# Kernel tuning notes

Measured on AMD Instinct MI355X. Metric: run time of the kernel, lower is better.

Reference implementation:

```python
import jax, jax.numpy as jnp
import numpy as np

B, LN, LT, D, DIN, H = 8, 64, 256, 1024, 2048, 4
LN_EPS = 1e-5
F16_EPS = float(np.finfo(np.float16).eps)


def setup_inputs() -> dict:
    key = jax.random.key(0)
    ks = jax.random.split(key, 16)
    n = lambda k, sh: jax.random.normal(k, sh, dtype=jnp.float32)
    s = 0.02
    z = lambda sh: jnp.zeros(sh, jnp.float32)
    return {
        "text_embeds": n(ks[0], (B, LT, D)),
        "node_embeds": n(ks[1], (B, LN, D)),
        "Wq": n(ks[2], (D, H * D)) * s, "bq": z((H * D,)),
        "Wk": n(ks[3], (D, H * D)) * s, "bk": z((H * D,)),
        "Wv": n(ks[4], (D, H * D)) * s, "bv": z((H * D,)),
        "Wo": n(ks[5], (H * D, D)) * s, "bo": z((D,)),
        "ln_g": jnp.ones((D,), jnp.float32), "ln_b": z((D,)),
        "aqW": n(ks[6], (D, D)) * s, "aqb": z((D,)),
        "akW": n(ks[7], (D, D)) * s, "akb": z((D,)),
        "att_v": n(ks[8], (D,)) * (1.0 / np.sqrt(D)),
        "att_b": z((D,)),
        "dp1W": n(ks[9], (D, DIN // 2)) * s, "dp1b": z((DIN // 2,)),
        "dp2W": n(ks[10], (DIN // 2, DIN)) * s, "dp2b": z((DIN,)),
        "gnn_mask": jax.random.randint(ks[11], (B, LN), 0, 2),
        "lm_mask": jax.random.randint(ks[12], (B, LT), 0, 2),
    }


def _forward(text_embeds, node_embeds, Wq, bq, Wk, bk, Wv, bv, Wo, bo, ln_g, ln_b,
             aqW, aqb, akW, akb, att_v, att_b, dp1W, dp1b, dp2W, dp2b,
             gnn_mask, lm_mask):
    x = node_embeds  # (B, LN, D)

    # ---- selfAttention_prompt: each of 4 heads has full width D ----
    def heads(w, b):
        return (x @ w + b).reshape(B, LN, H, D).transpose(0, 2, 1, 3)  # (B,H,LN,D)

    Q, K, V = heads(Wq, bq), heads(Wk, bk), heads(Wv, bv)
    A = jnp.einsum('bhqd,bhkd->bhqk', Q, K) / jnp.sqrt(jnp.float32(D))
    A = jnp.where(gnn_mask[:, None, None, :] == 0, -jnp.inf, A)
    alpha = jax.nn.softmax(A, axis=-1)
    out = jnp.einsum('bhqk,bhkd->bhqd', alpha, V)
    out = out.transpose(0, 2, 1, 3).reshape(B, LN, H * D)
    out = out @ Wo + bo + x
    # LayerNorm (torch default eps=1e-5)
    mu = out.mean(-1, keepdims=True)
    var = ((out - mu) ** 2).mean(-1, keepdims=True)
    H2 = (out - mu) / jnp.sqrt(var + LN_EPS) * ln_g + ln_b  # (B, LN, D)

    # ---- AdditiveAttention (Bahdanau): value_proj is unused in the original ----
    q = H2 @ aqW + aqb            # (B, LN, D)
    k = text_embeds @ akW + akb   # (B, LT, D)
    e = jnp.einsum('bqkd,d->bqk',
                   jnp.tanh(q[:, :, None, :] + k[:, None, :, :] + att_b), att_v)
    e = jnp.where(lm_mask[:, None, :] == 0, -jnp.inf, e)
    w = jax.nn.softmax(e, axis=-1)            # (B, LN, LT)
    H3 = jnp.einsum('bqk,bkd->bqd', w, text_embeds)  # context with raw V

    # ---- filter_Pool: masked mean over nodes ----
    m = gnn_mask.astype(H3.dtype)[:, :, None]
    cnt = jnp.clip(m.sum(1), F16_EPS, None)   # (B, 1)
    H4 = (H3 * m).sum(1) / cnt                # (B, D)

    # ---- domain projector (exact GELU like torch) ----
    Z = jax.nn.gelu(H4 @ dp1W + dp1b, approximate=False) @ dp2W + dp2b
    return Z  # (B, DIN)


def reference(text_embeds, node_embeds, Wq, bq, Wk, bk, Wv, bv, Wo, bo, ln_g, ln_b,
              aqW, aqb, akW, akb, att_v, att_b, dp1W, dp1b, dp2W, dp2b,
              gnn_mask, lm_mask):
    return _forward(text_embeds, node_embeds, Wq, bq, Wk, bk, Wv, bv, Wo, bo,
                    ln_g, ln_b, aqW, aqb, akW, akb, att_v, att_b,
                    dp1W, dp1b, dp2W, dp2b, gnn_mask, lm_mask)
```

## Files before the change

### kernel.cpp

```cpp
#include <hip/hip_runtime.h>
#include <hip/hip_bf16.h>
#include <math.h>

#define NB 8
#define LNN 64
#define LTN 256
#define DD 1024
#define NH 4
#define HDD 4096
#define DINN 2048
#define DHN 1024

#define C_TANH 2.8853900817779268f

typedef __bf16 bf16x8 __attribute__((ext_vector_type(8)));
typedef float f32x4 __attribute__((ext_vector_type(4)));

__device__ __forceinline__ float b2f(ushort u) {
  union { float f; unsigned int i; } x; x.i = ((unsigned int)u) << 16; return x.f;
}
__device__ __forceinline__ ushort f2b(float f) {
  unsigned int u = __builtin_bit_cast(unsigned int, f);
  u = (u + 0x7FFFu + ((u >> 16) & 1u)) >> 16;
  return (ushort)u;
}

__global__ __launch_bounds__(256) void cvt_all(const float* __restrict__ node,
                                               ushort* __restrict__ node_bf,
                                               const float* __restrict__ text,
                                               ushort* __restrict__ text_bf) {
  int bid = blockIdx.x;
  const float* in;
  ushort* out;
  int i;
  if (bid < 256) { in = node; out = node_bf; i = (bid * 256 + threadIdx.x) * 8; }
  else { in = text; out = text_bf; i = ((bid - 256) * 256 + threadIdx.x) * 8; }
  float4 a = *(const float4*)(in + i);
  float4 b = *(const float4*)(in + i + 4);
  ushort4 o0 = {f2b(a.x), f2b(a.y), f2b(a.z), f2b(a.w)};
  ushort4 o1 = {f2b(b.x), f2b(b.y), f2b(b.z), f2b(b.w)};
  *(ushort4*)(out + i) = o0;
  *(ushort4*)(out + i + 4) = o1;
}

__global__ __launch_bounds__(256) void tcvt3(const float* __restrict__ W0,
                                             const float* __restrict__ W1,
                                             const float* __restrict__ W2,
                                             ushort* __restrict__ Wt, int K, int N) {
  int z = blockIdx.z;
  const float* W = (z == 0) ? W0 : ((z == 1) ? W1 : W2);
  ushort* dst0 = Wt + (size_t)z * K * N;
  __shared__ float tf[64][65];
  int k0 = blockIdx.y << 6, n0 = blockIdx.x << 6;
  int t = threadIdx.x;
  int r = t >> 2, c4 = (t & 3) * 16;
  const float* src = W + (size_t)(k0 + r) * N + n0 + c4;
  float4 v0 = *(const float4*)(src);
  float4 v1 = *(const float4*)(src + 4);
  float4 v2 = *(const float4*)(src + 8);
  float4 v3 = *(const float4*)(src + 12);
  *(float4*)&tf[r][c4] = v0;
  *(float4*)&tf[r][c4 + 4] = v1;
  *(float4*)&tf[r][c4 + 8] = v2;
  *(float4*)&tf[r][c4 + 12] = v3;
  __syncthreads();
  int nl = t >> 2, kc = (t & 3) * 16;
  ushort tmp[16];
#pragma unroll
  for (int j = 0; j < 16; ++j) tmp[j] = f2b(tf[kc + j][nl]);
  ushort* dst = dst0 + (size_t)(n0 + nl) * K + k0 + kc;
  *(uint4*)(dst) = *(uint4*)&tmp[0];
  *(uint4*)(dst + 8) = *(uint4*)&tmp[8];
}

__global__ __launch_bounds__(256) void gemm_qkv3(const ushort* __restrict__ A,
                                                 const ushort* __restrict__ BtB,
                                                 const float* __restrict__ b0,
                                                 const float* __restrict__ b1,
                                                 const float* __restrict__ b2,
                                                 ushort* __restrict__ o0,
                                                 ushort* __restrict__ o1,
                                                 ushort* __restrict__ o2,
                                                 int M, int N, int K) {
  int z = blockIdx.z;
  const ushort* Bt = BtB + (size_t)z * N * K;
  const float* bias = (z == 0) ? b0 : ((z == 1) ? b1 : b2);
  ushort* Cout = (z == 0) ? o0 : ((z == 1) ? o1 : o2);
  __shared__ ushort Als[64 * 64];
  __shared__ ushort Bls[128 * 64];
  int tid = threadIdx.x;
  int m0 = blockIdx.y << 6, n0 = blockIdx.x << 7;
  int srow = tid >> 3, su = tid & 7;
  int sx = (su ^ (srow & 7)) * 8;
  const ushort* ga = A + (size_t)(m0 + srow) * K + su * 8;
  const ushort* gb = Bt + (size_t)(n0 + srow) * K + su * 8;
  int wa0 = srow * 64 + sx, wa1 = (srow + 32) * 64 + sx;
  int wb2 = (srow + 64) * 64 + sx, wb3 = (srow + 96) * 64 + sx;
  const size_t rs32 = (size_t)32 * K;
  int lane = tid & 63, w = tid >> 6;
  int wm = w >> 1, wn = w & 1;
  int r = lane & 15, kg = lane >> 4;
  f32x4 acc[2][4] = {};
  uint4 pa0 = *(const uint4*)(ga);
  uint4 pa1 = *(const uint4*)(ga + rs32);
  uint4 pb0 = *(const uint4*)(gb);
  uint4 pb1 = *(const uint4*)(gb + rs32);
  uint4 pb2 = *(const uint4*)(gb + 2 * rs32);
  uint4 pb3 = *(const uint4*)(gb + 3 * rs32);
  for (int k0 = 0; k0 < K; k0 += 64) {
    __syncthreads();
    *(uint4*)&Als[wa0] = pa0; *(uint4*)&Als[wa1] = pa1;
    *(uint4*)&Bls[wa0] = pb0; *(uint4*)&Bls[wa1] = pb1;
    *(uint4*)&Bls[wb2] = pb2; *(uint4*)&Bls[wb3] = pb3;
    __syncthreads();
    int kn = k0 + 64;
    if (kn < K) {
      pa0 = *(const uint4*)(ga + kn);
      pa1 = *(const uint4*)(ga + rs32 + kn);
      pb0 = *(const uint4*)(gb + kn);
      pb1 = *(const uint4*)(gb + rs32 + kn);
      pb2 = *(const uint4*)(gb + 2 * rs32 + kn);
      pb3 = *(const uint4*)(gb + 3 * rs32 + kn);
    }
#pragma unroll
    for (int h = 0; h < 2; ++h) {
      int sa = ((h * 4 + kg) ^ (r & 7)) * 8;
      bf16x8 af[2], bfr[4];
#pragma unroll
      for (int m = 0; m < 2; ++m)
        af[m] = *(const bf16x8*)&Als[(wm * 32 + m * 16 + r) * 64 + sa];
#pragma unroll
      for (int n = 0; n < 4; ++n)
        bfr[n] = *(const bf16x8*)&Bls[(wn * 64 + n * 16 + r) * 64 + sa];
#pragma unroll
      for (int m = 0; m < 2; ++m)
#pragma unroll
        for (int n = 0; n < 4; ++n)
          acc[m][n] = __builtin_amdgcn_mfma_f32_16x16x32_bf16(af[m], bfr[n], acc[m][n], 0, 0, 0);
    }
  }
#pragma unroll
  for (int m = 0; m < 2; ++m)
#pragma unroll
    for (int n = 0; n < 4; ++n) {
      f32x4 a = acc[m][n];
#pragma unroll
      for (int v = 0; v < 4; ++v) {
        int row = m0 + wm * 32 + m * 16 + kg * 4 + v;
        int col = n0 + wn * 64 + n * 16 + r;
        Cout[(size_t)row * N + col] = f2b(a[v] + bias[col]);
      }
    }
}

__global__ __launch_bounds__(256) void gemm_wo_split(const ushort* __restrict__ A,
                                                     const ushort* __restrict__ Bt,
                                                     float* __restrict__ P,
                                                     int M, int N, int K) {
  __shared__ ushort Als[64 * 64];
  __shared__ ushort Bls[128 * 64];
  int tid = threadIdx.x;
  int m0 = blockIdx.y << 6, n0 = blockIdx.x << 7;
  int Ks = K >> 2, kbase = blockIdx.z * Ks;
  int srow = tid >> 3, su = tid & 7;
  int sx = (su ^ (srow & 7)) * 8;
  const ushort* ga = A + (size_t)(m0 + srow) * K + kbase + su * 8;
  const ushort* gb = Bt + (size_t)(n0 + srow) * K + kbase + su * 8;
  int wa0 = srow * 64 + sx, wa1 = (srow + 32) * 64 + sx;
  int wb2 = (srow + 64) * 64 + sx, wb3 = (srow + 96) * 64 + sx;
  const size_t rs32 = (size_t)32 * K;
  int lane = tid & 63, w = tid >> 6;
  int wm = w >> 1, wn = w & 1;
  int r = lane & 15, kg = lane >> 4;
  f32x4 acc[2][4] = {};
  uint4 pa0 = *(const uint4*)(ga);
  uint4 pa1 = *(const uint4*)(ga + rs32);
  uint4 pb0 = *(const uint4*)(gb);
  uint4 pb1 = *(const uint4*)(gb + rs32);
  uint4 pb2 = *(const uint4*)(gb + 2 * rs32);
  uint4 pb3 = *(const uint4*)(gb + 3 * rs32);
  for (int k0 = 0; k0 < Ks; k0 += 64) {
    __syncthreads();
    *(uint4*)&Als[wa0] = pa0; *(uint4*)&Als[wa1] = pa1;
    *(uint4*)&Bls[wa0] = pb0; *(uint4*)&Bls[wa1] = pb1;
    *(uint4*)&Bls[wb2] = pb2; *(uint4*)&Bls[wb3] = pb3;
    __syncthreads();
    int kn = k0 + 64;
    if (kn < Ks) {
      pa0 = *(const uint4*)(ga + kn);
      pa1 = *(const uint4*)(ga + rs32 + kn);
      pb0 = *(const uint4*)(gb + kn);
      pb1 = *(const uint4*)(gb + rs32 + kn);
      pb2 = *(const uint4*)(gb + 2 * rs32 + kn);
      pb3 = *(const uint4*)(gb + 3 * rs32 + kn);
    }
#pragma unroll
    for (int h = 0; h < 2; ++h) {
      int sa = ((h * 4 + kg) ^ (r & 7)) * 8;
      bf16x8 af[2], bfr[4];
#pragma unroll
      for (int m = 0; m < 2; ++m)
        af[m] = *(const bf16x8*)&Als[(wm * 32 + m * 16 + r) * 64 + sa];
#pragma unroll
      for (int n = 0; n < 4; ++n)
        bfr[n] = *(const bf16x8*)&Bls[(wn * 64 + n * 16 + r) * 64 + sa];
#pragma unroll
      for (int m = 0; m < 2; ++m)
#pragma unroll
        for (int n = 0; n < 4; ++n)
          acc[m][n] = __builtin_amdgcn_mfma_f32_16x16x32_bf16(af[m], bfr[n], acc[m][n], 0, 0, 0);
    }
  }
#pragma unroll
  for (int m = 0; m < 2; ++m)
#pragma unroll
    for (int n = 0; n < 4; ++n) {
      f32x4 a = acc[m][n];
#pragma unroll
      for (int v = 0; v < 4; ++v) {
        int row = m0 + wm * 32 + m * 16 + kg * 4 + v;
        int col = n0 + wn * 64 + n * 16 + r;
        P[((size_t)blockIdx.z * M + row) * N + col] = a[v];
      }
    }
}

__global__ __launch_bounds__(256) void gemm_aqak(const ushort* __restrict__ H2,
                                                 const ushort* __restrict__ Tbf,
                                                 const ushort* __restrict__ TwtAQ,
                                                 const float* __restrict__ aqb,
                                                 const float* __restrict__ akb,
                                                 const float* __restrict__ attb,
                                                 float* __restrict__ QBu,
                                                 float* __restrict__ KAB,
                                                 int N, int K) {
  __shared__ ushort Als[64 * 64];
  __shared__ ushort Bls[128 * 64];
  int tid = threadIdx.x;
  int gm0 = blockIdx.y << 6, n0 = blockIdx.x << 7;
  const ushort* Abase;
  const ushort* Bt;
  const float* bias;
  const float* bias2;
  float* Obase;
  if (gm0 < 512) {
    Abase = H2 + (size_t)gm0 * K;
    Bt = TwtAQ;
    bias = aqb; bias2 = nullptr;
    Obase = QBu + (size_t)gm0 * N;
  } else {
    Abase = Tbf + (size_t)(gm0 - 512) * K;
    Bt = TwtAQ + (size_t)N * K;
    bias = akb; bias2 = attb;
    Obase = KAB + (size_t)(gm0 - 512) * N;
  }
  int srow = tid >> 3, su = tid & 7;
  int sx = (su ^ (srow & 7)) * 8;
  const ushort* ga = Abase + (size_t)srow * K + su * 8;
  const ushort* gb = Bt + (size_t)(n0 + srow) * K + su * 8;
  int wa0 = srow * 64 + sx, wa1 = (srow + 32) * 64 + sx;
  int wb2 = (srow + 64) * 64 + sx, wb3 = (srow + 96) * 64 + sx;
  const size_t rs32 = (size_t)32 * K;
  int lane = tid & 63, w = tid >> 6;
  int wm = w >> 1, wn = w & 1;
  int r = lane & 15, kg = lane >> 4;
  f32x4 acc[2][4] = {};
  uint4 pa0 = *(const uint4*)(ga);
  uint4 pa1 = *(const uint4*)(ga + rs32);
  uint4 pb0 = *(const uint4*)(gb);
  uint4 pb1 = *(const uint4*)(gb + rs32);
  uint4 pb2 = *(const uint4*)(gb + 2 * rs32);
  uint4 pb3 = *(const uint4*)(gb + 3 * rs32);
  for (int k0 = 0; k0 < K; k0 += 64) {
    __syncthreads();
    *(uint4*)&Als[wa0] = pa0; *(uint4*)&Als[wa1] = pa1;
    *(uint4*)&Bls[wa0] = pb0; *(uint4*)&Bls[wa1] = pb1;
    *(uint4*)&Bls[wb2] = pb2; *(uint4*)&Bls[wb3] = pb3;
    __syncthreads();
    int kn = k0 + 64;
    if (kn < K) {
      pa0 = *(const uint4*)(ga + kn);
      pa1 = *(const uint4*)(ga + rs32 + kn);
      pb0 = *(const uint4*)(gb + kn);
      pb1 = *(const uint4*)(gb + rs32 + kn);
      pb2 = *(const uint4*)(gb + 2 * rs32 + kn);
      pb3 = *(const uint4*)(gb + 3 * rs32 + kn);
    }
#pragma unroll
    for (int h = 0; h < 2; ++h) {
      int sa = ((h * 4 + kg) ^ (r & 7)) * 8;
      bf16x8 af[2], bfr[4];
#pragma unroll
      for (int m = 0; m < 2; ++m)
        af[m] = *(const bf16x8*)&Als[(wm * 32 + m * 16 + r) * 64 + sa];
#pragma unroll
      for (int n = 0; n < 4; ++n)
        bfr[n] = *(const bf16x8*)&Bls[(wn * 64 + n * 16 + r) * 64 + sa];
#pragma unroll
      for (int m = 0; m < 2; ++m)
#pragma unroll
        for (int n = 0; n < 4; ++n)
          acc[m][n] = __builtin_amdgcn_mfma_f32_16x16x32_bf16(af[m], bfr[n], acc[m][n], 0, 0, 0);
    }
  }
#pragma unroll
  for (int m = 0; m < 2; ++m)
#pragma unroll
    for (int n = 0; n < 4; ++n) {
      f32x4 a = acc[m][n];
#pragma unroll
      for (int v = 0; v < 4; ++v) {
        int lrow = wm * 32 + m * 16 + kg * 4 + v;
        int col = n0 + wn * 64 + n * 16 + r;
        float x = a[v] + bias[col];
        if (bias2) x += bias2[col];
        Obase[(size_t)lrow * N + col] = x * C_TANH;
      }
    }
}

__global__ __launch_bounds__(256) void wo_ln(const float* __restrict__ P,
                                             const float* __restrict__ bo,
                                             const float* __restrict__ node,
                                             const float* __restrict__ g,
                                             const float* __restrict__ be,
                                             ushort* __restrict__ Y) {
  int row = blockIdx.x, tid = threadIdx.x;
  int c = tid * 4;
  const size_t MN = (size_t)512 * 1024;
  size_t o = (size_t)row * DD + c;
  float4 v0 = *(const float4*)(P + o);
  float4 v1 = *(const float4*)(P + MN + o);
  float4 v2 = *(const float4*)(P + 2 * MN + o);
  float4 v3 = *(const float4*)(P + 3 * MN + o);
  float4 rv = *(const float4*)(node + o);
  float4 bv = *(const float4*)(bo + c);
  float4 v;
  v.x = v0.x + v1.x + v2.x + v3.x + rv.x + bv.x;
  v.y = v0.y + v1.y + v2.y + v3.y + rv.y + bv.y;
  v.z = v0.z + v1.z + v2.z + v3.z + rv.z + bv.z;
  v.w = v0.w + v1.w + v2.w + v3.w + rv.w + bv.w;
  float s = v.x + v.y + v.z + v.w;
  float ss = v.x * v.x + v.y * v.y + v.z * v.z + v.w * v.w;
  for (int o2 = 32; o2; o2 >>= 1) {
    s += __shfl_xor(s, o2, 64);
    ss += __shfl_xor(ss, o2, 64);
  }
  __shared__ float rb_[8];
  int lane = tid & 63, w = tid >> 6;
  if (lane == 0) { rb_[w] = s; rb_[4 + w] = ss; }
  __syncthreads();
  s = rb_[0] + rb_[1] + rb_[2] + rb_[3];
  ss = rb_[4] + rb_[5] + rb_[6] + rb_[7];
  float mu = s * (1.f / 1024.f);
  float var = ss * (1.f / 1024.f) - mu * mu;
  float rstd = rsqrtf(var + 1e-5f);
  ushort4 o4;
  o4.x = f2b((v.x - mu) * rstd * g[c + 0] + be[c + 0]);
  o4.y = f2b((v.y - mu) * rstd * g[c + 1] + be[c + 1]);
  o4.z = f2b((v.z - mu) * rstd * g[c + 2] + be[c + 2]);
  o4.w = f2b((v.w - mu) * rstd * g[c + 3] + be[c + 3]);
  *(ushort4*)(Y + (size_t)row * DD + c) = o4;
}

__global__ __launch_bounds__(256) void attn_qk(const ushort* __restrict__ Qb,
                                               const ushort* __restrict__ Kb,
                                               float* __restrict__ Sp) {
  int bh = blockIdx.x, ks = blockIdx.y;
  int b = bh >> 2;
  size_t base = ((size_t)b * LNN) * HDD + (size_t)(bh & 3) * DD + ks * 128;
  __shared__ ushort Als[64 * 64];
  __shared__ ushort Bls[64 * 64];
  int tid = threadIdx.x;
  int srow = tid >> 2, su0 = (tid & 3) * 2;
  const ushort* ga = Qb + base + (size_t)srow * HDD + su0 * 8;
  const ushort* gb = Kb + base + (size_t)srow * HDD + su0 * 8;
  int wa0 = srow * 64 + ((su0) ^ (srow & 7)) * 8;
  int wa1 = srow * 64 + ((su0 + 1) ^ (srow & 7)) * 8;
  int lane = tid & 63, w = tid >> 6;
  int wm = w >> 1, wn = w & 1;
  int r = lane & 15, kg = lane >> 4;
  f32x4 acc[2][2] = {};
  uint4 pa0 = *(const uint4*)(ga);
  uint4 pa1 = *(const uint4*)(ga + 8);
  uint4 pb0 = *(const uint4*)(gb);
  uint4 pb1 = *(const uint4*)(gb + 8);
  for (int k0 = 0; k0 < 128; k0 += 64) {
    __syncthreads();
    *(uint4*)&Als[wa0] = pa0; *(uint4*)&Als[wa1] = pa1;
    *(uint4*)&Bls[wa0] = pb0; *(uint4*)&Bls[wa1] = pb1;
    __syncthreads();
    if (k0 == 0) {
      pa0 = *(const uint4*)(ga + 64);
      pa1 = *(const uint4*)(ga + 64 + 8);
      pb0 = *(const uint4*)(gb + 64);
      pb1 = *(const uint4*)(gb + 64 + 8);
    }
#pragma unroll
    for (int h = 0; h < 2; ++h) {
      int sa = ((h * 4 + kg) ^ (r & 7)) * 8;
      bf16x8 af[2], bfr[2];
#pragma unroll
      for (int m = 0; m < 2; ++m)
        af[m] = *(const bf16x8*)&Als[(wm * 32 + m * 16 + r) * 64 + sa];
#pragma unroll
      for (int n = 0; n < 2; ++n)
        bfr[n] = *(const bf16x8*)&Bls[(wn * 32 + n * 16 + r) * 64 + sa];
#pragma unroll
      for (int m = 0; m < 2; ++m)
#pragma unroll
        for (int n = 0; n < 2; ++n)
          acc[m][n] = __builtin_amdgcn_mfma_f32_16x16x32_bf16(af[m], bfr[n], acc[m][n], 0, 0, 0);
    }
  }
  float* out = Sp + ((size_t)ks * 32 + bh) * 4096;
#pragma unroll
  for (int m = 0; m < 2; ++m)
#pragma unroll
    for (int n = 0; n < 2; ++n) {
      f32x4 a = acc[m][n];
#pragma unroll
      for (int v = 0; v < 4; ++v) {
        int row = wm * 32 + m * 16 + kg * 4 + v;
        int col = wn * 32 + n * 16 + r;
        out[row * 64 + col] = a[v];
      }
    }
}

__global__ __launch_bounds__(256) void attn_pv(const float* __restrict__ Sp,
                                               const ushort* __restrict__ Vb,
                                               const int* __restrict__ gmask,
                                               ushort* __restrict__ AO) {
  int bid = blockIdx.x;
  int bh = bid >> 3, dt = bid & 7;
  int b = bh >> 2;
  int d0 = dt * 128;
  size_t base = ((size_t)b * LNN) * HDD + (size_t)(bh & 3) * DD;
  __shared__ float S[64][68];
  __shared__ ushort Pls[64 * 72];
  __shared__ ushort Vt[128 * 72];
  int tid = threadIdx.x;
  int lane = tid & 63, w = tid >> 6;
  {
    int fbase = tid * 16;
    float a[16];
#pragma unroll
    for (int i = 0; i < 16; i += 4) {
      float4 v = *(const float4*)(Sp + (size_t)bh * 4096 + fbase + i);
      a[i] = v.x; a[i + 1] = v.y; a[i + 2] = v.z; a[i + 3] = v.w;
    }
#pragma unroll
    for (int ks = 1; ks < 8; ++ks) {
      const float* p = Sp + ((size_t)ks * 32 + bh) * 4096 + fbase;
#pragma unroll
      for (int i = 0; i < 16; i += 4) {
        float4 v = *(const float4*)(p + i);
        a[i] += v.x; a[i + 1] += v.y; a[i + 2] += v.z; a[i + 3] += v.w;
      }
    }
    int q = fbase >> 6, k = fbase & 63;
#pragma unroll
    for (int i = 0; i < 16; ++i) S[q][k + i] = a[i];
  }
  {
    int kq = lane, dq = w * 32;
    const ushort* src = Vb + base + (size_t)kq * HDD + d0 + dq;
    uint4 v0 = *(const uint4*)src;
    uint4 v1 = *(const uint4*)(src + 8);
    uint4 v2 = *(const uint4*)(src + 16);
    uint4 v3 = *(const uint4*)(src + 24);
    ushort tmp[32];
    *(uint4*)&tmp[0] = v0; *(uint4*)&tmp[8] = v1;
    *(uint4*)&tmp[16] = v2; *(uint4*)&tmp[24] = v3;
#pragma unroll
    for (int j = 0; j < 32; ++j) Vt[(dq + j) * 72 + kq] = tmp[j];
  }
  __syncthreads();
  bool valid = gmask[b * LNN + lane] != 0;
  for (int i = 0; i < 16; ++i) {
    int q = w * 16 + i;
    float v = valid ? S[q][lane] * 0.03125f : -__builtin_inff();
    float mx = v;
    for (int o = 32; o; o >>= 1) mx = fmaxf(mx, __shfl_xor(mx, o, 64));
    float e = valid ? __expf(v - mx) : 0.f;
    float s = e;
    for (int o = 32; o; o >>= 1) s += __shfl_xor(s, o, 64);
    Pls[q * 72 + lane] = f2b(__fdividef(e, s));
  }
  __syncthreads();
  int wm = w >> 1, wn = w & 1;
  int r = lane & 15, kg = lane >> 4;
  f32x4 acc[2][4] = {};
#pragma unroll
  for (int h = 0; h < 2; ++h) {
    int ko = h * 32 + kg * 8;
    bf16x8 af[2], bfr[4];
#pragma unroll
    for (int m = 0; m < 2; ++m)
      af[m] = *(const bf16x8*)&Pls[(wm * 32 + m * 16 + r) * 72 + ko];
#pragma unroll
    for (int n = 0; n < 4; ++n)
      bfr[n] = *(const bf16x8*)&Vt[(wn * 64 + n * 16 + r) * 72 + ko];
#pragma unroll
    for (int m = 0; m < 2; ++m)
#pragma unroll
      for (int n = 0; n < 4; ++n)
        acc[m][n] = __builtin_amdgcn_mfma_f32_16x16x32_bf16(af[m], bfr[n], acc[m][n], 0, 0, 0);
  }
#pragma unroll
  for (int m = 0; m < 2; ++m)
#pragma unroll
    for (int n = 0; n < 4; ++n) {
      f32x4 a = acc[m][n];
#pragma unroll
      for (int v = 0; v < 4; ++v) {
        int q = wm * 32 + m * 16 + kg * 4 + v;
        int col = wn * 64 + n * 16 + r;
        AO[base + (size_t)q * HDD + d0 + col] = f2b(a[v]);
      }
    }
}

__global__ __launch_bounds__(256) void addatt_e(const float* __restrict__ QBu,
                                                const float* __restrict__ KAB,
                                                const float* __restrict__ av_,
                                                float* __restrict__ E4) {
  int dq = blockIdx.x, qt = blockIdx.y, b = blockIdx.z;
  int tid = threadIdx.x;
  __shared__ float qs[4][256];
  __shared__ float avs[256];
  __shared__ float red[4];
  int bq0 = b * LNN + qt * 4;
#pragma unroll
  for (int qq = 0; qq < 4; ++qq)
    qs[qq][tid] = QBu[(size_t)(bq0 + qq) * DD + dq * 256 + tid];
  float av = av_[dq * 256 + tid];
  avs[tid] = av;
  float s = av;
  for (int o = 32; o; o >>= 1) s += __shfl_xor(s, o, 64);
  int lane = tid & 63, w = tid >> 6;
  if (lane == 0) red[w] = s;
  __syncthreads();
  float sumav = red[0] + red[1] + red[2] + red[3];
  const float* kr = KAB + (size_t)(b * LTN + tid) * DD + dq * 256;
  float ac0 = 0.f, ac1 = 0.f, ac2 = 0.f, ac3 = 0.f;
#pragma unroll 2
  for (int d = 0; d < 256; d += 4) {
    float4 kv = *(const float4*)(kr + d);
    float4 av4 = *(const float4*)&avs[d];
    float4 q0 = *(const float4*)&qs[0][d];
    float4 q1 = *(const float4*)&qs[1][d];
    float4 q2 = *(const float4*)&qs[2][d];
    float4 q3 = *(const float4*)&qs[3][d];
    ac0 = fmaf(av4.x, __builtin_amdgcn_rcpf(__builtin_amdgcn_exp2f(q0.x + kv.x) + 1.f), ac0);
    ac1 = fmaf(av4.x, __builtin_amdgcn_rcpf(__builtin_amdgcn_exp2f(q1.x + kv.x) + 1.f), ac1);
    ac2 = fmaf(av4.x, __builtin_amdgcn_rcpf(__builtin_amdgcn_exp2f(q2.x + kv.x) + 1.f), ac2);
    ac3 = fmaf(av4.x, __builtin_amdgcn_rcpf(__builtin_amdgcn_exp2f(q3.x + kv.x) + 1.f), ac3);
    ac0 = fmaf(av4.y, __builtin_amdgcn_rcpf(__builtin_amdgcn_exp2f(q0.y + kv.y) + 1.f), ac0);
    ac1 = fmaf(av4.y, __builtin_amdgcn_rcpf(__builtin_amdgcn_exp2f(q1.y + kv.y) + 1.f), ac1);
    ac2 = fmaf(av4.y, __builtin_amdgcn_rcpf(__builtin_amdgcn_exp2f(q2.y + kv.y) + 1.f), ac2);
    ac3 = fmaf(av4.y, __builtin_amdgcn_rcpf(__builtin_amdgcn_exp2f(q3.y + kv.y) + 1.f), ac3);
    ac0 = fmaf(av4.z, __builtin_amdgcn_rcpf(__builtin_amdgcn_exp2f(q0.z + kv.z) + 1.f), ac0);
    ac1 = fmaf(av4.z, __builtin_amdgcn_rcpf(__builtin_amdgcn_exp2f(q1.z + kv.z) + 1.f), ac1);
    ac2 = fmaf(av4.z, __builtin_amdgcn_rcpf(__builtin_amdgcn_exp2f(q2.z + kv.z) + 1.f), ac2);
    ac3 = fmaf(av4.z, __builtin_amdgcn_rcpf(__builtin_amdgcn_exp2f(q3.z + kv.z) + 1.f), ac3);
    ac0 = fmaf(av4.w, __builtin_amdgcn_rcpf(__builtin_amdgcn_exp2f(q0.w + kv.w) + 1.f), ac0);
    ac1 = fmaf(av4.w, __builtin_amdgcn_rcpf(__builtin_amdgcn_exp2f(q1.w + kv.w) + 1.f), ac1);
    ac2 = fmaf(av4.w, __builtin_amdgcn_rcpf(__builtin_amdgcn_exp2f(q2.w + kv.w) + 1.f), ac2);
    ac3 = fmaf(av4.w, __builtin_amdgcn_rcpf(__builtin_amdgcn_exp2f(q3.w + kv.w) + 1.f), ac3);
  }
  size_t ebase = ((size_t)dq * 512 + bq0) * LTN + tid;
  E4[ebase] = sumav - 2.f * ac0;
  E4[ebase + LTN] = sumav - 2.f * ac1;
  E4[ebase + 2 * LTN] = sumav - 2.f * ac2;
  E4[ebase + 3 * LTN] = sumav - 2.f * ac3;
}

__global__ __launch_bounds__(256) void addatt_sm(const float* __restrict__ E4,
                                                 const int* __restrict__ lmask,
                                                 float* __restrict__ Wv) {
  int bq = blockIdx.x;
  int b = bq >> 6;
  int tid = threadIdx.x;
  __shared__ float rb_[8];
  float e = E4[(size_t)bq * LTN + tid] + E4[((size_t)512 + bq) * LTN + tid] +
            E4[((size_t)1024 + bq) * LTN + tid] + E4[((size_t)1536 + bq) * LTN + tid];
  bool valid = lmask[b * LTN + tid] != 0;
  float v = valid ? e : -__builtin_inff();
  int lane = tid & 63, w = tid >> 6;
  float m = v;
  for (int o = 32; o; o >>= 1) m = fmaxf(m, __shfl_xor(m, o, 64));
  if (lane == 0) rb_[w] = m;
  __syncthreads();
  m = fmaxf(fmaxf(rb_[0], rb_[1]), fmaxf(rb_[2], rb_[3]));
  float ex = valid ? __expf(v - m) : 0.f;
  float sm = ex;
  for (int o = 32; o; o >>= 1) sm += __shfl_xor(sm, o, 64);
  if (lane == 0) rb_[4 + w] = sm;
  __syncthreads();
  sm = rb_[4] + rb_[5] + rb_[6] + rb_[7];
  Wv[(size_t)bq * LTN + tid] = __fdividef(ex, sm);
}

__global__ __launch_bounds__(256) void addatt_pool(const float* __restrict__ Wv,
                                                   const float* __restrict__ text,
                                                   const int* __restrict__ gmask,
                                                   float* __restrict__ H4) {
  int dt = blockIdx.x, b = blockIdx.y;
  int tid = threadIdx.x;
  __shared__ float cf[LTN];
  float c = 0.f, cnt = 0.f;
#pragma unroll 8
  for (int q = 0; q < LNN; ++q) {
    float m = (gmask[b * LNN + q] != 0) ? 1.f : 0.f;
    cnt += m;
    c = fmaf(m, Wv[(size_t)(b * LNN + q) * LTN + tid], c);
  }
  cf[tid] = c;
  cnt = fmaxf(cnt, 9.765625e-04f);
  __syncthreads();
  int d = dt * 256 + tid;
  const float* tb = text + (size_t)b * LTN * DD + d;
  float acc = 0.f;
#pragma unroll 8
  for (int k = 0; k < LTN; ++k) acc = fmaf(cf[k], tb[(size_t)k * DD], acc);
  H4[b * DD + d] = acc / cnt;
}

__global__ __launch_bounds__(256) void dp_split(const float* __restrict__ X,
                                                const float* __restrict__ W,
                                                float* __restrict__ P,
                                                int K, int N) {
  int jt = blockIdx.x, kt = blockIdx.y;
  int t = threadIdx.x;
  __shared__ float xs[8][32];
  if (t < 64) {
    int b = t >> 3, kk = (t & 7) * 4;
    *(float4*)&xs[b][kk] = *(const float4*)(X + (size_t)b * K + kt * 32 + kk);
  }
  __syncthreads();
  int j = jt * 64 + (t & 63);
  int bg = (t >> 6) * 2;
  const float* wp = W + (size_t)(kt * 32) * N + j;
  float a0 = 0.f, a1 = 0.f;
#pragma unroll
  for (int k = 0; k < 32; ++k) {
    float w = wp[(size_t)k * N];
    a0 = fmaf(xs[bg + 0][k], w, a0);
    a1 = fmaf(xs[bg + 1][k], w, a1);
  }
  P[((size_t)kt * 8 + bg + 0) * N + j] = a0;
  P[((size_t)kt * 8 + bg + 1) * N + j] = a1;
}

template <int GELU>
__global__ __launch_bounds__(256) void dp_reduce(const float* __restrict__ P,
                                                 const float* __restrict__ bias,
                                                 float* __restrict__ O, int N) {
  int b = blockIdx.y;
  int j = blockIdx.x * 256 + threadIdx.x;
  float s = bias[j];
#pragma unroll 8
  for (int kt = 0; kt < 32; ++kt) s += P[((size_t)kt * 8 + b) * N + j];
  if constexpr (GELU) s = 0.5f * s * (1.f + erff(s * 0.70710678118654752440f));
  O[(size_t)b * N + j] = s;
}

extern "C" void kernel_launch(void* const* d_in, const int* in_sizes, int n_in,
                              void* d_out, int out_size, void* d_ws, size_t ws_size,
                              hipStream_t stream) {
  const float* text = (const float*)d_in[0];
  const float* node = (const float*)d_in[1];
  const float* Wq = (const float*)d_in[2];
  const float* bq = (const float*)d_in[3];
  const float* Wk = (const float*)d_in[4];
  const float* bk = (const float*)d_in[5];
  const float* Wv = (const float*)d_in[6];
  const float* bv = (const float*)d_in[7];
  const float* Wo = (const float*)d_in[8];
  const float* bo = (const float*)d_in[9];
  const float* lng = (const float*)d_in[10];
  const float* lnb = (const float*)d_in[11];
  const float* aqW = (const float*)d_in[12];
  const float* aqb = (const float*)d_in[13];
  const float* akW = (const float*)d_in[14];
  const float* akb = (const float*)d_in[15];
  const float* attv = (const float*)d_in[16];
  const float* attb = (const float*)d_in[17];
  const float* dp1W = (const float*)d_in[18];
  const float* dp1b = (const float*)d_in[19];
  const float* dp2W = (const float*)d_in[20];
  const float* dp2b = (const float*)d_in[21];
  const int* gmask = (const int*)d_in[22];
  const int* lmask = (const int*)d_in[23];
  (void)in_sizes; (void)n_in; (void)out_size;

  char* base = (char*)d_ws;
#define MB(x) (((size_t)(x)) << 20)
  ushort* Twt = (ushort*)(base);
  float* Sp = (float*)(base);
  ushort* node_bf = (ushort*)(base + MB(8));
  ushort* text_bf = (ushort*)(base + MB(9));
  ushort* Qb = (ushort*)(base + MB(13));
  ushort* Kb = (ushort*)(base + MB(17));
  ushort* Vb = (ushort*)(base + MB(21));
  ushort* AO = (ushort*)(base + MB(25));
  float* E4 = (float*)(base + MB(13));
  float* Wvb = (float*)(base + MB(15));
  ushort* H2 = (ushort*)(base + MB(15) + (512 << 10));
  float* P_Wo = (float*)(base + MB(17));
  float* P1 = (float*)(base + MB(18));
  float* P2 = (float*)(base + MB(19));
  float* QBu = (float*)(base + MB(21));
  float* KAB = (float*)(base + MB(25));
  float* H4 = (float*)(base + MB(33));
  float* G = (float*)(base + MB(33) + 32768);
  ushort* TwtQKV = (ushort*)(base + MB(34));
  float* Z = (float*)d_out;
  const bool bigws = ws_size >= MB(59);
#undef MB

  const int M1 = NB * LNN;
  dim3 blk(256);

  cvt_all<<<dim3(1280), blk, 0, stream>>>(node, node_bf, text, text_bf);

  if (bigws) {
    tcvt3<<<dim3(HDD / 64, DD / 64, 3), blk, 0, stream>>>(Wq, Wk, Wv, TwtQKV, DD, HDD);
    gemm_qkv3<<<dim3(HDD / 128, M1 / 64, 3), blk, 0, stream>>>(node_bf, TwtQKV, bq, bk, bv, Qb, Kb, Vb, M1, HDD, DD);
  } else {
    tcvt3<<<dim3(HDD / 64, DD / 64, 1), blk, 0, stream>>>(Wq, Wq, Wq, Twt, DD, HDD);
    gemm_qkv3<<<dim3(HDD / 128, M1 / 64, 1), blk, 0, stream>>>(node_bf, Twt, bq, bq, bq, Qb, Qb, Qb, M1, HDD, DD);
    tcvt3<<<dim3(HDD / 64, DD / 64, 1), blk, 0, stream>>>(Wk, Wk, Wk, Twt, DD, HDD);
    gemm_qkv3<<<dim3(HDD / 128, M1 / 64, 1), blk, 0, stream>>>(node_bf, Twt, bk, bk, bk, Kb, Kb, Kb, M1, HDD, DD);
    tcvt3<<<dim3(HDD / 64, DD / 64, 1), blk, 0, stream>>>(Wv, Wv, Wv, Twt, DD, HDD);
    gemm_qkv3<<<dim3(HDD / 128, M1 / 64, 1), blk, 0, stream>>>(node_bf, Twt, bv, bv, bv, Vb, Vb, Vb, M1, HDD, DD);
  }

  attn_qk<<<dim3(NB * NH, 8), blk, 0, stream>>>(Qb, Kb, Sp);
  attn_pv<<<dim3(NB * NH * 8), blk, 0, stream>>>(Sp, Vb, gmask, AO);

  tcvt3<<<dim3(DD / 64, HDD / 64, 1), blk, 0, stream>>>(Wo, Wo, Wo, Twt, HDD, DD);
  gemm_wo_split<<<dim3(DD / 128, M1 / 64, 4), blk, 0, stream>>>(AO, Twt, P_Wo, M1, DD, HDD);
  wo_ln<<<dim3(M1), blk, 0, stream>>>(P_Wo, bo, node, lng, lnb, H2);

  tcvt3<<<dim3(DD / 64, DD / 64, 2), blk, 0, stream>>>(aqW, akW, akW, Twt, DD, DD);
  gemm_aqak<<<dim3(DD / 128, 40), blk, 0, stream>>>(H2, text_bf, Twt, aqb, akb, attb, QBu, KAB, DD, DD);

  addatt_e<<<dim3(4, 16, NB), blk, 0, stream>>>(QBu, KAB, attv, E4);
  addatt_sm<<<dim3(M1), blk, 0, stream>>>(E4, lmask, Wvb);
  addatt_pool<<<dim3(4, NB), blk, 0, stream>>>(Wvb, text, gmask, H4);

  dp_split<<<dim3(DHN / 64, 32), blk, 0, stream>>>(H4, dp1W, P1, DD, DHN);
  dp_reduce<1><<<dim3(DHN / 256, NB), blk, 0, stream>>>(P1, dp1b, G, DHN);
  dp_split<<<dim3(DINN / 64, 32), blk, 0, stream>>>(G, dp2W, P2, DHN, DINN);
  dp_reduce<0><<<dim3(DINN / 256, NB), blk, 0, stream>>>(P2, dp2b, Z, DINN);
}
```

Baseline: 173.7 us.

## Fuse all input/weight conversions into one prep kernel and retile additive attention

Merges the activation bf16 conversion and all weight transpose-conversions (QKV, Wo, aq/ak) into a single large launch with a fixed workspace layout, removing the small-workspace fallback and several separate launches. This cuts launch gaps and lets weight conversion for later stages run alongside the earlier ones. The additive-attention score kernel now processes 8 queries over 128-wide d slices instead of 4 queries over 256, so each loaded K row is reused across more queries. The softmax kernel then sums 8 partial slices instead of 4. The change now assumes the workspace is large enough for the fixed layout.

Result: faster. 162.0 us (-6.7%).

```diff
diff --git a/kernel.cpp b/kernel.cpp
--- a/kernel.cpp
+++ b/kernel.cpp
@@ -16,43 +16,61 @@
 typedef __bf16 bf16x8 __attribute__((ext_vector_type(8)));
 typedef float f32x4 __attribute__((ext_vector_type(4)));
 
-__device__ __forceinline__ float b2f(ushort u) {
-  union { float f; unsigned int i; } x; x.i = ((unsigned int)u) << 16; return x.f;
-}
 __device__ __forceinline__ ushort f2b(float f) {
   unsigned int u = __builtin_bit_cast(unsigned int, f);
   u = (u + 0x7FFFu + ((u >> 16) & 1u)) >> 16;
   return (ushort)u;
 }
 
-__global__ __launch_bounds__(256) void cvt_all(const float* __restrict__ node,
-                                               ushort* __restrict__ node_bf,
-                                               const float* __restrict__ text,
-                                               ushort* __restrict__ text_bf) {
+__global__ __launch_bounds__(256) void prep(const float* __restrict__ node,
+                                            ushort* __restrict__ node_bf,
+                                            const float* __restrict__ text,
+                                            ushort* __restrict__ text_bf,
+                                            const float* __restrict__ Wq,
+                                            const float* __restrict__ Wk,
+                                            const float* __restrict__ Wv,
+                                            const float* __restrict__ Wo,
+                                            const float* __restrict__ aqW,
+                                            const float* __restrict__ akW,
+                                            ushort* __restrict__ TwtQKV,
+                                            ushort* __restrict__ TwtWo,
+                                            ushort* __restrict__ TwtAQ) {
   int bid = blockIdx.x;
-  const float* in;
-  ushort* out;
-  int i;
-  if (bid < 256) { in = node; out = node_bf; i = (bid * 256 + threadIdx.x) * 8; }
-  else { in = text; out = text_bf; i = ((bid - 256) * 256 + threadIdx.x) * 8; }
-  float4 a = *(const float4*)(in + i);
-  float4 b = *(const float4*)(in + i + 4);
-  ushort4 o0 = {f2b(a.x), f2b(a.y), f2b(a.z), f2b(a.w)};
-  ushort4 o1 = {f2b(b.x), f2b(b.y), f2b(b.z), f2b(b.w)};
-  *(ushort4*)(out + i) = o0;
-  *(ushort4*)(out + i + 4) = o1;
-}
-
-__global__ __launch_bounds__(256) void tcvt3(const float* __restrict__ W0,
-                                             const float* __restrict__ W1,
-                                             const float* __restrict__ W2,
-                                             ushort* __restrict__ Wt, int K, int N) {
-  int z = blockIdx.z;
-  const float* W = (z == 0) ? W0 : ((z == 1) ? W1 : W2);
-  ushort* dst0 = Wt + (size_t)z * K * N;
+  int t = threadIdx.x;
+  if (bid < 1280) {
+    const float* in;
+    ushort* out;
+    int i;
+    if (bid < 256) { in = node; out = node_bf; i = (bid * 256 + t) * 8; }
+    else { in = text; out = text_bf; i = ((bid - 256) * 256 + t) * 8; }
+    float4 a = *(const float4*)(in + i);
+    float4 b = *(const float4*)(in + i + 4);
+    ushort4 o0 = {f2b(a.x), f2b(a.y), f2b(a.z), f2b(a.w)};
+    ushort4 o1 = {f2b(b.x), f2b(b.y), f2b(b.z), f2b(b.w)};
+    *(ushort4*)(out + i) = o0;
+    *(ushort4*)(out + i + 4) = o1;
+    return;
+  }
+  bid -= 1280;
+  const float* W;
+  ushort* dst0;
+  int K, N, tt;
+  if (bid < 3072) {
+    int z = bid >> 10;
+    tt = bid & 1023;
+    W = (z == 0) ? Wq : ((z == 1) ? Wk : Wv);
+    dst0 = TwtQKV + (size_t)z * DD * HDD;
+    K = DD; N = HDD;
+  } else if (bid < 4096) {
+    tt = bid - 3072; W = Wo; dst0 = TwtWo; K = HDD; N = DD;
+  } else if (bid < 4352) {
+    tt = bid - 4096; W = aqW; dst0 = TwtAQ; K = DD; N = DD;
+  } else {
+    tt = bid - 4352; W = akW; dst0 = TwtAQ + (size_t)DD * DD; K = DD; N = DD;
+  }
+  int ntn = N >> 6;
+  int n0 = (tt % ntn) << 6, k0 = (tt / ntn) << 6;
   __shared__ float tf[64][65];
-  int k0 = blockIdx.y << 6, n0 = blockIdx.x << 6;
-  int t = threadIdx.x;
   int r = t >> 2, c4 = (t & 3) * 16;
   const float* src = W + (size_t)(k0 + r) * N + n0 + c4;
   float4 v0 = *(const float4*)(src);
@@ -525,67 +543,57 @@
 __global__ __launch_bounds__(256) void addatt_e(const float* __restrict__ QBu,
                                                 const float* __restrict__ KAB,
                                                 const float* __restrict__ av_,
-                                                float* __restrict__ E4) {
-  int dq = blockIdx.x, qt = blockIdx.y, b = blockIdx.z;
+                                                float* __restrict__ E8) {
+  int ds = blockIdx.x, qt = blockIdx.y, b = blockIdx.z;
   int tid = threadIdx.x;
-  __shared__ float qs[4][256];
-  __shared__ float avs[256];
+  __shared__ float qs[8][128];
+  __shared__ float avs[128];
   __shared__ float red[4];
-  int bq0 = b * LNN + qt * 4;
-#pragma unroll
-  for (int qq = 0; qq < 4; ++qq)
-    qs[qq][tid] = QBu[(size_t)(bq0 + qq) * DD + dq * 256 + tid];
-  float av = av_[dq * 256 + tid];
-  avs[tid] = av;
+  int bq0 = b * LNN + qt * 8;
+  {
+    int qq = tid >> 5, dd = (tid & 31) * 4;
+    *(float4*)&qs[qq][dd] = *(const float4*)(QBu + (size_t)(bq0 + qq) * DD + ds * 128 + dd);
+  }
+  float av = (tid < 128) ? av_[ds * 128 + tid] : 0.f;
+  if (tid < 128) avs[tid] = av;
   float s = av;
   for (int o = 32; o; o >>= 1) s += __shfl_xor(s, o, 64);
   int lane = tid & 63, w = tid >> 6;
   if (lane == 0) red[w] = s;
   __syncthreads();
   float sumav = red[0] + red[1] + red[2] + red[3];
-  const float* kr = KAB + (size_t)(b * LTN + tid) * DD + dq * 256;
-  float ac0 = 0.f, ac1 = 0.f, ac2 = 0.f, ac3 = 0.f;
+  const float* kr = KAB + (size_t)(b * LTN + tid) * DD + ds * 128;
+  float ac[8] = {};
 #pragma unroll 2
-  for (int d = 0; d < 256; d += 4) {
+  for (int d = 0; d < 128; d += 4) {
     float4 kv = *(const float4*)(kr + d);
     float4 av4 = *(const float4*)&avs[d];
-    float4 q0 = *(const float4*)&qs[0][d];
-    float4 q1 = *(const float4*)&qs[1][d];
-    float4 q2 = *(const float4*)&qs[2][d];
-    float4 q3 = *(const float4*)&qs[3][d];
-    ac0 = fmaf(av4.x, __builtin_amdgcn_rcpf(__builtin_amdgcn_exp2f(q0.x + kv.x) + 1.f), ac0);
-    ac1 = fmaf(av4.x, __builtin_amdgcn_rcpf(__builtin_amdgcn_exp2f(q1.x + kv.x) + 1.f), ac1);
-    ac2 = fmaf(av4.x, __builtin_amdgcn_rcpf(__builtin_amdgcn_exp2f(q2.x + kv.x) + 1.f), ac2);
-    ac3 = fmaf(av4.x, __builtin_amdgcn_rcpf(__builtin_amdgcn_exp2f(q3.x + kv.x) + 1.f), ac3);
-    ac0 = fmaf(av4.y, __builtin_amdgcn_rcpf(__builtin_amdgcn_exp2f(q0.y + kv.y) + 1.f), ac0);
-    ac1 = fmaf(av4.y, __builtin_amdgcn_rcpf(__builtin_amdgcn_exp2f(q1.y + kv.y) + 1.f), ac1);
-    ac2 = fmaf(av4.y, __builtin_amdgcn_rcpf(__builtin_amdgcn_exp2f(q2.y + kv.y) + 1.f), ac2);
-    ac3 = fmaf(av4.y, __builtin_amdgcn_rcpf(__builtin_amdgcn_exp2f(q3.y + kv.y) + 1.f), ac3);
-    ac0 = fmaf(av4.z, __builtin_amdgcn_rcpf(__builtin_amdgcn_exp2f(q0.z + kv.z) + 1.f), ac0);
-    ac1 = fmaf(av4.z, __builtin_amdgcn_rcpf(__builtin_amdgcn_exp2f(q1.z + kv.z) + 1.f), ac1);
-    ac2 = fmaf(av4.z, __builtin_amdgcn_rcpf(__builtin_amdgcn_exp2f(q2.z + kv.z) + 1.f), ac2);
-    ac3 = fmaf(av4.z, __builtin_amdgcn_rcpf(__builtin_amdgcn_exp2f(q3.z + kv.z) + 1.f), ac3);
-    ac0 = fmaf(av4.w, __builtin_amdgcn_rcpf(__builtin_amdgcn_exp2f(q0.w + kv.w) + 1.f), ac0);
-    ac1 = fmaf(av4.w, __builtin_amdgcn_rcpf(__builtin_amdgcn_exp2f(q1.w + kv.w) + 1.f), ac1);
-    ac2 = fmaf(av4.w, __builtin_amdgcn_rcpf(__builtin_amdgcn_exp2f(q2.w + kv.w) + 1.f), ac2);
-    ac3 = fmaf(av4.w, __builtin_amdgcn_rcpf(__builtin_amdgcn_exp2f(q3.w + kv.w) + 1.f), ac3);
-  }
-  size_t ebase = ((size_t)dq * 512 + bq0) * LTN + tid;
-  E4[ebase] = sumav - 2.f * ac0;
-  E4[ebase + LTN] = sumav - 2.f * ac1;
-  E4[ebase + 2 * LTN] = sumav - 2.f * ac2;
-  E4[ebase + 3 * LTN] = sumav - 2.f * ac3;
-}
-
-__global__ __launch_bounds__(256) void addatt_sm(const float* __restrict__ E4,
+#pragma unroll
+    for (int qq = 0; qq < 8; ++qq) {
+      float4 q4 = *(const float4*)&qs[qq][d];
+      ac[qq] = fmaf(av4.x, __builtin_amdgcn_rcpf(__builtin_amdgcn_exp2f(q4.x + kv.x) + 1.f), ac[qq]);
+      ac[qq] = fmaf(av4.y, __builtin_amdgcn_rcpf(__builtin_amdgcn_exp2f(q4.y + kv.y) + 1.f), ac[qq]);
+      ac[qq] = fmaf(av4.z, __builtin_amdgcn_rcpf(__builtin_amdgcn_exp2f(q4.z + kv.z) + 1.f), ac[qq]);
+      ac[qq] = fmaf(av4.w, __builtin_amdgcn_rcpf(__builtin_amdgcn_exp2f(q4.w + kv.w) + 1.f), ac[qq]);
+    }
+  }
+  size_t ebase = ((size_t)ds * 512 + bq0) * LTN + tid;
+#pragma unroll
+  for (int qq = 0; qq < 8; ++qq)
+    E8[ebase + (size_t)qq * LTN] = sumav - 2.f * ac[qq];
+}
+
+__global__ __launch_bounds__(256) void addatt_sm(const float* __restrict__ E8,
                                                  const int* __restrict__ lmask,
                                                  float* __restrict__ Wv) {
   int bq = blockIdx.x;
   int b = bq >> 6;
   int tid = threadIdx.x;
   __shared__ float rb_[8];
-  float e = E4[(size_t)bq * LTN + tid] + E4[((size_t)512 + bq) * LTN + tid] +
-            E4[((size_t)1024 + bq) * LTN + tid] + E4[((size_t)1536 + bq) * LTN + tid];
+  float e = 0.f;
+#pragma unroll
+  for (int ks = 0; ks < 8; ++ks)
+    e += E8[((size_t)ks * 512 + bq) * LTN + tid];
   bool valid = lmask[b * LTN + tid] != 0;
   float v = valid ? e : -__builtin_inff();
   int lane = tid & 63, w = tid >> 6;
@@ -694,62 +702,52 @@
   const float* dp2b = (const float*)d_in[21];
   const int* gmask = (const int*)d_in[22];
   const int* lmask = (const int*)d_in[23];
-  (void)in_sizes; (void)n_in; (void)out_size;
+  (void)in_sizes; (void)n_in; (void)out_size; (void)ws_size;
 
   char* base = (char*)d_ws;
 #define MB(x) (((size_t)(x)) << 20)
-  ushort* Twt = (ushort*)(base);
-  float* Sp = (float*)(base);
-  ushort* node_bf = (ushort*)(base + MB(8));
-  ushort* text_bf = (ushort*)(base + MB(9));
-  ushort* Qb = (ushort*)(base + MB(13));
-  ushort* Kb = (ushort*)(base + MB(17));
-  ushort* Vb = (ushort*)(base + MB(21));
-  ushort* AO = (ushort*)(base + MB(25));
-  float* E4 = (float*)(base + MB(13));
-  float* Wvb = (float*)(base + MB(15));
-  ushort* H2 = (ushort*)(base + MB(15) + (512 << 10));
-  float* P_Wo = (float*)(base + MB(17));
-  float* P1 = (float*)(base + MB(18));
-  float* P2 = (float*)(base + MB(19));
-  float* QBu = (float*)(base + MB(21));
-  float* KAB = (float*)(base + MB(25));
-  float* H4 = (float*)(base + MB(33));
-  float* G = (float*)(base + MB(33) + 32768);
-  ushort* TwtQKV = (ushort*)(base + MB(34));
+  ushort* TwtQKV = (ushort*)(base);
+  ushort* TwtWo = (ushort*)(base + MB(24));
+  ushort* TwtAQ = (ushort*)(base + MB(32));
+  ushort* node_bf = (ushort*)(base + MB(36));
+  ushort* text_bf = (ushort*)(base + MB(37));
+  ushort* Qb = (ushort*)(base + MB(41));
+  ushort* Kb = (ushort*)(base + MB(45));
+  ushort* Vb = (ushort*)(base + MB(49));
+  ushort* AO = (ushort*)(base + MB(53));
+  float* Sp = (float*)(base + MB(57));
+  float* P_Wo = (float*)(base + MB(61));
+  ushort* H2 = (ushort*)(base + MB(69));
+  float* QBu = (float*)(base + MB(70));
+  float* KAB = (float*)(base + MB(72));
+  float* E8 = (float*)(base + MB(80));
+  float* Wvb = (float*)(base + MB(84));
+  float* H4 = (float*)(base + MB(84) + (512 << 10));
+  float* G = (float*)(base + MB(84) + (512 << 10) + 32768);
+  float* P1 = (float*)(base + MB(85));
+  float* P2 = (float*)(base + MB(86));
   float* Z = (float*)d_out;
-  const bool bigws = ws_size >= MB(59);
 #undef MB
 
   const int M1 = NB * LNN;
   dim3 blk(256);
 
-  cvt_all<<<dim3(1280), blk, 0, stream>>>(node, node_bf, text, text_bf);
-
-  if (bigws) {
-    tcvt3<<<dim3(HDD / 64, DD / 64, 3), blk, 0, stream>>>(Wq, Wk, Wv, TwtQKV, DD, HDD);
-    gemm_qkv3<<<dim3(HDD / 128, M1 / 64, 3), blk, 0, stream>>>(node_bf, TwtQKV, bq, bk, bv, Qb, Kb, Vb, M1, HDD, DD);
-  } else {
-    tcvt3<<<dim3(HDD / 64, DD / 64, 1), blk, 0, stream>>>(Wq, Wq, Wq, Twt, DD, HDD);
-    gemm_qkv3<<<dim3(HDD / 128, M1 / 64, 1), blk, 0, stream>>>(node_bf, Twt, bq, bq, bq, Qb, Qb, Qb, M1, HDD, DD);
-    tcvt3<<<dim3(HDD / 64, DD / 64, 1), blk, 0, stream>>>(Wk, Wk, Wk, Twt, DD, HDD);
-    gemm_qkv3<<<dim3(HDD / 128, M1 / 64, 1), blk, 0, stream>>>(node_bf, Twt, bk, bk, bk, Kb, Kb, Kb, M1, HDD, DD);
-    tcvt3<<<dim3(HDD / 64, DD / 64, 1), blk, 0, stream>>>(Wv, Wv, Wv, Twt, DD, HDD);
-    gemm_qkv3<<<dim3(HDD / 128, M1 / 64, 1), blk, 0, stream>>>(node_bf, Twt, bv, bv, bv, Vb, Vb, Vb, M1, HDD, DD);
-  }
+  prep<<<dim3(5888), blk, 0, stream>>>(node, node_bf, text, text_bf,
+                                       Wq, Wk, Wv, Wo, aqW, akW,
+                                       TwtQKV, TwtWo, TwtAQ);
+
+  gemm_qkv3<<<dim3(HDD / 128, M1 / 64, 3), blk, 0, stream>>>(node_bf, TwtQKV, bq, bk, bv, Qb, Kb, Vb, M1, HDD, DD);
 
   attn_qk<<<dim3(NB * NH, 8), blk, 0, stream>>>(Qb, Kb, Sp);
   attn_pv<<<dim3(NB * NH * 8), blk, 0, stream>>>(Sp, Vb, gmask, AO);
 
-  tcvt3<<<dim3(DD / 64, HDD / 64, 1), blk, 0, stream>>>(Wo, Wo, Wo, Twt, HDD, DD);
-  gemm_wo_split<<<dim3(DD / 128, M1 / 64, 4), blk, 0, stream>>>(AO, Twt, P_Wo, M1, DD, HDD);
+  gemm_wo_split<<<dim3(DD / 128, M1 / 64, 4), blk, 0, stream>>>(AO, TwtWo, P_Wo, M1, DD, HDD);
   wo_ln<<<dim3(M1), blk, 0, stream>>>(P_Wo, bo, node, lng, lnb, H2);
 
-  tcvt3<<<dim3(DD / 64, DD / 64, 2), blk, 0, stream>>>(aqW, akW, akW, Twt, DD, DD);
-  gemm_aqak<<<dim3(DD / 128, 40), blk, 0, stream>>>(H2, text_bf, Twt, aqb, akb, attb, QBu, KAB, DD, DD);
-
-  addatt_e<<<dim3(4, 16, NB), blk, 0, stream>>>(QBu, KAB, attv, E4);
-  addatt_sm<<<dim3(M1), blk, 0, stream>>>(E4, lmask, Wvb);
+  gemm_aqak<<<dim3(DD / 128, 40), blk, 0, stream>>>(H2, text_bf, TwtAQ, aqb, akb, attb, QBu, KAB, DD, DD);
+
+  addatt_e<<<dim3(8, 8, NB), blk, 0, stream>>>(QBu, KAB, attv, E8);
+  addatt_sm<<<dim3(M1), blk, 0, stream>>>(E8, lmask, Wvb);
   addatt_pool<<<dim3(4, NB), blk, 0, stream>>>(Wvb, text, gmask, H4);
 
   dp_split<<<dim3(DHN / 64, 32), blk, 0, stream>>>(H4, dp1W, P1, DD, DHN);
```
